# Kernel optimization log

Measured on AMD Instinct MI355X. Metric: run time of the kernel, lower is better.

The kernel has to match this reference:

```python
import jax, jax.numpy as jnp
import numpy as np


def setup_inputs() -> dict:
    key = jax.random.key(0)
    k1, k2, k3, k4 = jax.random.split(key, 4)
    B, S, D = 2, 2048, 1024
    return {
        "X": jax.random.normal(k1, (B, S, D), dtype=jnp.float32),
        "W_q": jax.random.normal(k2, (D, D), dtype=jnp.float32),
        "W_k": jax.random.normal(k3, (D, D), dtype=jnp.float32),
        "W_v": jax.random.normal(k4, (D, D), dtype=jnp.float32),
        "n_heads": 16,
    }


def reference(X, W_q, W_k, W_v, n_heads):
    B, S, D = X.shape
    H = n_heads
    dh = D // H
    # QKV projections, split heads: [B,S,D] -> [H,B,S,dh]
    def split_heads(Y):
        return Y.reshape(B, S, H, dh).transpose(2, 0, 1, 3)
    Q = split_heads(X @ W_q)
    K = split_heads(X @ W_k)
    V = split_heads(X @ W_v)
    scale = 1.0 / jnp.sqrt(jnp.asarray(dh, dtype=X.dtype))
    # [H,B,S,S] attention scores (naive, matches the original)
    scores = jax.nn.softmax(jnp.einsum("hbqd,hbkd->hbqk", Q, K) * scale, axis=-1)
    out = jnp.einsum("hbqk,hbkd->hbqd", scores, V)  # [H,B,S,dh]
    # torch.concat(out, 0) over leading H dim -> [H*B, S, dh]
    return out.reshape(H * B, S, dh)
```

## Files before the change

### kernel.cpp

```cpp
#include <hip/hip_runtime.h>

typedef unsigned short u16;
typedef unsigned int u32;
typedef __bf16 bf16x8 __attribute__((ext_vector_type(8)));
typedef float f32x4 __attribute__((ext_vector_type(4)));

#define WT_HI_E  ((size_t)0)
#define WT_LO_E  ((size_t)3 << 20)
#define X_HI_E   ((size_t)6 << 20)
#define X_LO_E   ((size_t)10 << 20)
#define Q_HI_E   ((size_t)14 << 20)
#define Q_LO_E   ((size_t)18 << 20)
#define K_HI_E   ((size_t)22 << 20)
#define K_LO_E   ((size_t)26 << 20)
#define V_HI_E   ((size_t)30 << 20)

__device__ __forceinline__ u16 bf16_rne(float x) {
  u32 u = __float_as_uint(x);
  u32 r = (u + 0x7fffu + ((u >> 16) & 1u)) >> 16;
  return (u16)r;
}
__device__ __forceinline__ float bf16_f(u16 h) {
  return __uint_as_float(((u32)h) << 16);
}

__device__ __forceinline__ void gload16(const u16* g, u16* l) {
  __builtin_amdgcn_global_load_lds(
      (const __attribute__((address_space(1))) void*)g,
      (__attribute__((address_space(3))) void*)l, 16, 0, 0);
}

__global__ __launch_bounds__(256) void k_xsplit(const float* __restrict__ X,
                                                u16* __restrict__ ws) {
  u16* xh = ws + X_HI_E;
  u16* xl = ws + X_LO_E;
  size_t i = ((size_t)blockIdx.x * 256 + threadIdx.x) * 8;
  float4 a = *(const float4*)(X + i);
  float4 b = *(const float4*)(X + i + 4);
  float v[8] = {a.x, a.y, a.z, a.w, b.x, b.y, b.z, b.w};
  u32 Hh[4], Ll[4];
#pragma unroll
  for (int j = 0; j < 4; j++) {
    u16 h0 = bf16_rne(v[2 * j]);
    u16 l0 = bf16_rne(v[2 * j] - bf16_f(h0));
    u16 h1 = bf16_rne(v[2 * j + 1]);
    u16 l1 = bf16_rne(v[2 * j + 1] - bf16_f(h1));
    Hh[j] = (u32)h0 | ((u32)h1 << 16);
    Ll[j] = (u32)l0 | ((u32)l1 << 16);
  }
  *(uint4*)(xh + i) = make_uint4(Hh[0], Hh[1], Hh[2], Hh[3]);
  *(uint4*)(xl + i) = make_uint4(Ll[0], Ll[1], Ll[2], Ll[3]);
}

__global__ __launch_bounds__(256) void k_wsplit(const float* __restrict__ w0,
                                                const float* __restrict__ w1,
                                                const float* __restrict__ w2,
                                                u16* __restrict__ ws) {
  int z = blockIdx.z;
  const float* W = (z == 0) ? w0 : ((z == 1) ? w1 : w2);
  u16* th = ws + WT_HI_E + (size_t)z * (1u << 20);
  u16* tl = ws + WT_LO_E + (size_t)z * (1u << 20);
  __shared__ float tile[32][33];
  int bx = blockIdx.x * 32, by = blockIdx.y * 32;
  int tx = threadIdx.x & 31, ty = threadIdx.x >> 5;
#pragma unroll
  for (int i = 0; i < 4; i++) {
    int r = ty + i * 8;
    tile[r][tx] = W[(size_t)(by + r) * 1024 + bx + tx];
  }
  __syncthreads();
#pragma unroll
  for (int i = 0; i < 4; i++) {
    int r = ty + i * 8;
    float v = tile[tx][r];
    int n = bx + r, k = by + tx;
    u16 h = bf16_rne(v);
    u16 l = bf16_rne(v - bf16_f(h));
    th[(size_t)n * 1024 + k] = h;
    tl[(size_t)n * 1024 + k] = l;
  }
}

__global__ __launch_bounds__(256) void k_proj(u16* __restrict__ ws) {
  int z = blockIdx.z;
  const u16* Xh = ws + X_HI_E;
  const u16* Xl = ws + X_LO_E;
  const u16* Wh = ws + WT_HI_E + (size_t)z * (1u << 20);
  const u16* Wl = ws + WT_LO_E + (size_t)z * (1u << 20);
  u16* dsth = ws + ((z == 0) ? Q_HI_E : ((z == 1) ? K_HI_E : V_HI_E));
  u16* dstl = (z == 0) ? (ws + Q_LO_E) : ((z == 1) ? (ws + K_LO_E) : (u16*)0);

  __shared__ u16 sXh[4096], sXl[4096], sWh[4096], sWl[4096];
  int M0 = blockIdx.y * 128, N0 = blockIdx.x * 128;
  int tid = threadIdx.x, lane = tid & 63, w = tid >> 6;
  int quad = lane >> 4, l16 = lane & 15;
  int mb = (w & 1) * 64, nb = (w >> 1) * 64;

  const f32x4 z4 = {0.f, 0.f, 0.f, 0.f};
  f32x4 acc[4][4];
#pragma unroll
  for (int i = 0; i < 4; i++)
#pragma unroll
    for (int j = 0; j < 4; j++) acc[i][j] = z4;

  for (int kk = 0; kk < 1024; kk += 32) {
    __syncthreads();
#pragma unroll
    for (int c2 = 0; c2 < 2; c2++) {
      int cb = c2 * 256 + w * 64;
      int c = cb + lane;
      int row = c >> 2, q8 = c & 3;
      size_t gx = (size_t)(M0 + row) * 1024 + kk + q8 * 8;
      size_t gw = (size_t)(N0 + row) * 1024 + kk + q8 * 8;
      gload16(Xh + gx, sXh + (size_t)cb * 8);
      gload16(Wh + gw, sWh + (size_t)cb * 8);
      if (z != 2) {
        gload16(Xl + gx, sXl + (size_t)cb * 8);
        gload16(Wl + gw, sWl + (size_t)cb * 8);
      }
    }
    __syncthreads();
    bf16x8 ah[4], bh[4];
#pragma unroll
    for (int i = 0; i < 4; i++) {
      ah[i] = *(const bf16x8*)&sXh[(mb + i * 16 + l16) * 32 + quad * 8];
      bh[i] = *(const bf16x8*)&sWh[(nb + i * 16 + l16) * 32 + quad * 8];
    }
    if (z != 2) {
      bf16x8 al[4], bl[4];
#pragma unroll
      for (int i = 0; i < 4; i++) {
        al[i] = *(const bf16x8*)&sXl[(mb + i * 16 + l16) * 32 + quad * 8];
        bl[i] = *(const bf16x8*)&sWl[(nb + i * 16 + l16) * 32 + quad * 8];
      }
#pragma unroll
      for (int i = 0; i < 4; i++)
#pragma unroll
        for (int j = 0; j < 4; j++) {
          f32x4 c0 = acc[i][j];
          c0 = __builtin_amdgcn_mfma_f32_16x16x32_bf16(ah[i], bh[j], c0, 0, 0, 0);
          c0 = __builtin_amdgcn_mfma_f32_16x16x32_bf16(ah[i], bl[j], c0, 0, 0, 0);
          c0 = __builtin_amdgcn_mfma_f32_16x16x32_bf16(al[i], bh[j], c0, 0, 0, 0);
          acc[i][j] = c0;
        }
    } else {
#pragma unroll
      for (int i = 0; i < 4; i++)
#pragma unroll
        for (int j = 0; j < 4; j++)
          acc[i][j] = __builtin_amdgcn_mfma_f32_16x16x32_bf16(ah[i], bh[j], acc[i][j], 0, 0, 0);
    }
  }

  if (z == 2) {
#pragma unroll
    for (int i = 0; i < 4; i++)
#pragma unroll
      for (int j = 0; j < 4; j++) {
        int mg = M0 + mb + i * 16 + quad * 4;
        int ng = N0 + nb + j * 16 + l16;
        int b = mg >> 11, s = mg & 2047;
        int hh = ng >> 6, d = ng & 63;
        u16 p0 = bf16_rne(acc[i][j][0]);
        u16 p1 = bf16_rne(acc[i][j][1]);
        u16 p2 = bf16_rne(acc[i][j][2]);
        u16 p3 = bf16_rne(acc[i][j][3]);
        *(uint2*)&dsth[((size_t)(hh * 2 + b) * 64 + d) * 2048 + s] =
            make_uint2((u32)p0 | ((u32)p1 << 16), (u32)p2 | ((u32)p3 << 16));
      }
  } else {
    float qscale = (z == 0) ? 0.125f : 1.0f;
#pragma unroll
    for (int i = 0; i < 4; i++)
#pragma unroll
      for (int j = 0; j < 4; j++)
#pragma unroll
        for (int r = 0; r < 4; r++) {
          int mg = M0 + mb + i * 16 + quad * 4 + r;
          int ng = N0 + nb + j * 16 + l16;
          int b = mg >> 11, s = mg & 2047;
          int hh = ng >> 6, d = ng & 63;
          size_t idx = ((size_t)(hh * 2 + b) * 2048 + s) * 64 + d;
          float y = acc[i][j][r] * qscale;
          u16 h = bf16_rne(y);
          dsth[idx] = h;
          dstl[idx] = bf16_rne(y - bf16_f(h));
        }
  }
}

__global__ __launch_bounds__(256, 4) void k_attn(u16* __restrict__ ws,
                                                 float* __restrict__ out) {
  const u16* Qh = ws + Q_HI_E;
  const u16* Ql = ws + Q_LO_E;
  const u16* Kh = ws + K_HI_E;
  const u16* Kl = ws + K_LO_E;
  const u16* Vt = ws + V_HI_E;

  __shared__ u16 sKh[2][64][32], sKl[2][64][32], sVt[2][64][32];
  __shared__ u16 sP[4][16][72];

  int id = blockIdx.x;
  int hb = id & 31, qb = id >> 5;
  int q0 = qb * 64;

  int tid = threadIdx.x, w = tid >> 6, lane = tid & 63;
  int quad = lane >> 4, l16 = lane & 15;
  size_t base = (size_t)hb * (2048 * 64);
  int row0 = q0 + w * 16;

  bf16x8 qh[2], ql[2];
#pragma unroll
  for (int kc = 0; kc < 2; kc++) {
    size_t off = base + (size_t)(row0 + l16) * 64 + kc * 32 + quad * 8;
    qh[kc] = *(const bf16x8*)(Qh + off);
    ql[kc] = *(const bf16x8*)(Ql + off);
  }
  const f32x4 z4 = {0.f, 0.f, 0.f, 0.f};
  float mr = -1e30f, lr = 0.f;
  f32x4 o[4];
#pragma unroll
  for (int dn = 0; dn < 4; dn++) o[dn] = z4;

  int srow = w * 16 + (lane >> 2);
  int sch = lane & 3;

  for (int kt = 0; kt < 2048; kt += 64) {
    __syncthreads();
#pragma unroll
    for (int kc = 0; kc < 2; kc++) {
      size_t kg = base + (size_t)(kt + srow) * 64 + kc * 32 + sch * 8;
      gload16(Kh + kg, &sKh[kc][w * 16][0]);
      gload16(Kl + kg, &sKl[kc][w * 16][0]);
      size_t vg = base + (size_t)srow * 2048 + kt + kc * 32 + sch * 8;
      gload16(Vt + vg, &sVt[kc][w * 16][0]);
    }
    __syncthreads();

    f32x4 sc[4] = {z4, z4, z4, z4};
#pragma unroll
    for (int kc = 0; kc < 2; kc++) {
      bf16x8 kh[4], klo[4];
#pragma unroll
      for (int nt = 0; nt < 4; nt++) {
        kh[nt] = *(const bf16x8*)&sKh[kc][nt * 16 + l16][quad * 8];
        klo[nt] = *(const bf16x8*)&sKl[kc][nt * 16 + l16][quad * 8];
      }
#pragma unroll
      for (int nt = 0; nt < 4; nt++) {
        f32x4 a = sc[nt];
        a = __builtin_amdgcn_mfma_f32_16x16x32_bf16(kh[nt], qh[kc], a, 0, 0, 0);
        a = __builtin_amdgcn_mfma_f32_16x16x32_bf16(kh[nt], ql[kc], a, 0, 0, 0);
        a = __builtin_amdgcn_mfma_f32_16x16x32_bf16(klo[nt], qh[kc], a, 0, 0, 0);
        sc[nt] = a;
      }
    }
    float m1v = sc[0][0];
#pragma unroll
    for (int nt = 0; nt < 4; nt++)
#pragma unroll
      for (int r = 0; r < 4; r++) m1v = fmaxf(m1v, sc[nt][r]);
    m1v = fmaxf(m1v, __shfl_xor(m1v, 16));
    m1v = fmaxf(m1v, __shfl_xor(m1v, 32));
    float mnew = fmaxf(mr, m1v);
    float alpha = __expf(mr - mnew);
    mr = mnew;
    float rs = 0.f;
#pragma unroll
    for (int nt = 0; nt < 4; nt++) {
      float p0 = __expf(sc[nt][0] - mnew);
      float p1 = __expf(sc[nt][1] - mnew);
      float p2 = __expf(sc[nt][2] - mnew);
      float p3 = __expf(sc[nt][3] - mnew);
      rs += (p0 + p1) + (p2 + p3);
      *(uint2*)&sP[w][l16][nt * 16 + quad * 4] =
          make_uint2((u32)bf16_rne(p0) | ((u32)bf16_rne(p1) << 16),
                     (u32)bf16_rne(p2) | ((u32)bf16_rne(p3) << 16));
    }
    rs += __shfl_xor(rs, 16);
    rs += __shfl_xor(rs, 32);
    lr = lr * alpha + rs;
    float af[4];
#pragma unroll
    for (int r = 0; r < 4; r++) af[r] = __shfl(alpha, quad * 20 + r);
#pragma unroll
    for (int dn = 0; dn < 4; dn++)
#pragma unroll
      for (int r = 0; r < 4; r++) o[dn][r] *= af[r];
#pragma unroll
    for (int kc = 0; kc < 2; kc++) {
      bf16x8 pa = *(const bf16x8*)&sP[w][l16][kc * 32 + quad * 8];
#pragma unroll
      for (int dn = 0; dn < 4; dn++) {
        bf16x8 vb = *(const bf16x8*)&sVt[kc][dn * 16 + l16][quad * 8];
        o[dn] = __builtin_amdgcn_mfma_f32_16x16x32_bf16(pa, vb, o[dn], 0, 0, 0);
      }
    }
  }

  float lf[4];
#pragma unroll
  for (int r = 0; r < 4; r++) lf[r] = __shfl(lr, quad * 20 + r);
#pragma unroll
  for (int r = 0; r < 4; r++) {
    int row = row0 + quad * 4 + r;
    size_t g = (size_t)hb * 2048 + row;
    float inv = 1.f / lf[r];
#pragma unroll
    for (int dn = 0; dn < 4; dn++) out[g * 64 + dn * 16 + l16] = o[dn][r] * inv;
  }
}

extern "C" void kernel_launch(void* const* d_in, const int* in_sizes, int n_in,
                              void* d_out, int out_size, void* d_ws, size_t ws_size,
                              hipStream_t stream) {
  const float* X = (const float*)d_in[0];
  const float* Wq = (const float*)d_in[1];
  const float* Wk = (const float*)d_in[2];
  const float* Wv = (const float*)d_in[3];
  u16* ws = (u16*)d_ws;
  float* out = (float*)d_out;

  k_xsplit<<<dim3(2048), dim3(256), 0, stream>>>(X, ws);
  k_wsplit<<<dim3(32, 32, 3), dim3(256), 0, stream>>>(Wq, Wk, Wv, ws);
  k_proj<<<dim3(8, 32, 3), dim3(256), 0, stream>>>(ws);
  k_attn<<<dim3(1024), dim3(256), 0, stream>>>(ws, out);
}
```

Baseline: 263.6 us.

## Rework attention kernel with 32x32 MFMA, swizzled K/V layout and double-buffered staging

The attention kernel now gives each wave 32 query rows and uses 32x32x16 MFMA tiles, doubling the query tile per block and halving the grid. The probability tile stays in registers, exchanged between lane halves with cross-lane shuffles, so the shared-memory round trip for P goes away. K/V tiles are double-buffered so the next tile's loads overlap compute, and one barrier per iteration remains. The projection kernel writes K and V^T in an XOR-swizzled layout to avoid LDS bank conflicts on reads. The trade-offs are higher register pressure (launch bounds lowered to 2 blocks/SM), fewer blocks, and P rounding done by simple add-and-truncate.

```diff
diff --git a/kernel.cpp b/kernel.cpp
--- a/kernel.cpp
+++ b/kernel.cpp
@@ -4,6 +4,7 @@
 typedef unsigned int u32;
 typedef __bf16 bf16x8 __attribute__((ext_vector_type(8)));
 typedef float f32x4 __attribute__((ext_vector_type(4)));
+typedef float f32x16 __attribute__((ext_vector_type(16)));
 
 #define WT_HI_E  ((size_t)0)
 #define WT_LO_E  ((size_t)3 << 20)
@@ -161,11 +162,13 @@
         int ng = N0 + nb + j * 16 + l16;
         int b = mg >> 11, s = mg & 2047;
         int hh = ng >> 6, d = ng & 63;
+        int cp = ((s >> 3) & 7) ^ (d & 7);
+        int ssw = (s & ~63) | (cp << 3) | (s & 7);
         u16 p0 = bf16_rne(acc[i][j][0]);
         u16 p1 = bf16_rne(acc[i][j][1]);
         u16 p2 = bf16_rne(acc[i][j][2]);
         u16 p3 = bf16_rne(acc[i][j][3]);
-        *(uint2*)&dsth[((size_t)(hh * 2 + b) * 64 + d) * 2048 + s] =
+        *(uint2*)&dsth[((size_t)(hh * 2 + b) * 64 + d) * 2048 + ssw] =
             make_uint2((u32)p0 | ((u32)p1 << 16), (u32)p2 | ((u32)p3 << 16));
       }
   } else {
@@ -180,7 +183,9 @@
           int ng = N0 + nb + j * 16 + l16;
           int b = mg >> 11, s = mg & 2047;
           int hh = ng >> 6, d = ng & 63;
-          size_t idx = ((size_t)(hh * 2 + b) * 2048 + s) * 64 + d;
+          int d2 = d;
+          if (z == 1) d2 = ((((d >> 3) ^ (s & 7)) & 7) << 3) | (d & 7);
+          size_t idx = ((size_t)(hh * 2 + b) * 2048 + s) * 64 + d2;
           float y = acc[i][j][r] * qscale;
           u16 h = bf16_rne(y);
           dsth[idx] = h;
@@ -189,7 +194,7 @@
   }
 }
 
-__global__ __launch_bounds__(256, 4) void k_attn(u16* __restrict__ ws,
+__global__ __launch_bounds__(256, 2) void k_attn(u16* __restrict__ ws,
                                                  float* __restrict__ out) {
   const u16* Qh = ws + Q_HI_E;
   const u16* Ql = ws + Q_LO_E;
@@ -197,118 +202,127 @@
   const u16* Kl = ws + K_LO_E;
   const u16* Vt = ws + V_HI_E;
 
-  __shared__ u16 sKh[2][64][32], sKl[2][64][32], sVt[2][64][32];
-  __shared__ u16 sP[4][16][72];
+  __shared__ u16 sKh[2][64][64], sKl[2][64][64], sVt[2][64][64];
 
   int id = blockIdx.x;
   int hb = id & 31, qb = id >> 5;
-  int q0 = qb * 64;
-
   int tid = threadIdx.x, w = tid >> 6, lane = tid & 63;
-  int quad = lane >> 4, l16 = lane & 15;
+  int l31 = lane & 31, h = lane >> 5;
   size_t base = (size_t)hb * (2048 * 64);
-  int row0 = q0 + w * 16;
-
-  bf16x8 qh[2], ql[2];
-#pragma unroll
-  for (int kc = 0; kc < 2; kc++) {
-    size_t off = base + (size_t)(row0 + l16) * 64 + kc * 32 + quad * 8;
-    qh[kc] = *(const bf16x8*)(Qh + off);
-    ql[kc] = *(const bf16x8*)(Ql + off);
-  }
-  const f32x4 z4 = {0.f, 0.f, 0.f, 0.f};
+  int qw0 = qb * 128 + w * 32;
+
+  int srow = lane >> 3, sch = lane & 7;
+
+  auto stage = [&](int buf, int kt) {
+#pragma unroll
+    for (int b2 = 0; b2 < 2; b2++) {
+      int rr = w * 16 + b2 * 8;
+      size_t kg = base + (size_t)(kt + rr + srow) * 64 + sch * 8;
+      gload16(Kh + kg, &sKh[buf][rr][0]);
+      gload16(Kl + kg, &sKl[buf][rr][0]);
+      size_t vg = base + (size_t)(rr + srow) * 2048 + kt + sch * 8;
+      gload16(Vt + vg, &sVt[buf][rr][0]);
+    }
+  };
+
+  stage(0, 0);
+
+  bf16x8 qh[4], ql[4];
+#pragma unroll
+  for (int ks = 0; ks < 4; ks++) {
+    size_t off = base + (size_t)(qw0 + l31) * 64 + ks * 16 + h * 8;
+    qh[ks] = *(const bf16x8*)(Qh + off);
+    ql[ks] = *(const bf16x8*)(Ql + off);
+  }
+
+  f32x16 o[2];
+#pragma unroll
+  for (int i = 0; i < 16; i++) { o[0][i] = 0.f; o[1][i] = 0.f; }
   float mr = -1e30f, lr = 0.f;
-  f32x4 o[4];
-#pragma unroll
-  for (int dn = 0; dn < 4; dn++) o[dn] = z4;
-
-  int srow = w * 16 + (lane >> 2);
-  int sch = lane & 3;
-
-  for (int kt = 0; kt < 2048; kt += 64) {
+
+  auto rdA = [&](const u16 t[64][64], int mt, int ks) -> bf16x8 {
+    int ch = ((ks * 2 + h) ^ (l31 & 7)) * 8;
+    return *(const bf16x8*)&t[mt * 32 + l31][ch];
+  };
+
+  for (int it = 0; it < 32; it++) {
     __syncthreads();
-#pragma unroll
-    for (int kc = 0; kc < 2; kc++) {
-      size_t kg = base + (size_t)(kt + srow) * 64 + kc * 32 + sch * 8;
-      gload16(Kh + kg, &sKh[kc][w * 16][0]);
-      gload16(Kl + kg, &sKl[kc][w * 16][0]);
-      size_t vg = base + (size_t)srow * 2048 + kt + kc * 32 + sch * 8;
-      gload16(Vt + vg, &sVt[kc][w * 16][0]);
-    }
-    __syncthreads();
-
-    f32x4 sc[4] = {z4, z4, z4, z4};
-#pragma unroll
-    for (int kc = 0; kc < 2; kc++) {
-      bf16x8 kh[4], klo[4];
-#pragma unroll
-      for (int nt = 0; nt < 4; nt++) {
-        kh[nt] = *(const bf16x8*)&sKh[kc][nt * 16 + l16][quad * 8];
-        klo[nt] = *(const bf16x8*)&sKl[kc][nt * 16 + l16][quad * 8];
-      }
-#pragma unroll
-      for (int nt = 0; nt < 4; nt++) {
-        f32x4 a = sc[nt];
-        a = __builtin_amdgcn_mfma_f32_16x16x32_bf16(kh[nt], qh[kc], a, 0, 0, 0);
-        a = __builtin_amdgcn_mfma_f32_16x16x32_bf16(kh[nt], ql[kc], a, 0, 0, 0);
-        a = __builtin_amdgcn_mfma_f32_16x16x32_bf16(klo[nt], qh[kc], a, 0, 0, 0);
-        sc[nt] = a;
-      }
-    }
-    float m1v = sc[0][0];
-#pragma unroll
-    for (int nt = 0; nt < 4; nt++)
-#pragma unroll
-      for (int r = 0; r < 4; r++) m1v = fmaxf(m1v, sc[nt][r]);
-    m1v = fmaxf(m1v, __shfl_xor(m1v, 16));
-    m1v = fmaxf(m1v, __shfl_xor(m1v, 32));
-    float mnew = fmaxf(mr, m1v);
+    if (it + 1 < 32) stage((it + 1) & 1, (it + 1) * 64);
+    int buf = it & 1;
+
+    f32x16 sc[2];
+#pragma unroll
+    for (int i = 0; i < 16; i++) { sc[0][i] = 0.f; sc[1][i] = 0.f; }
+#pragma unroll
+    for (int ks = 0; ks < 4; ks++)
+#pragma unroll
+      for (int mt = 0; mt < 2; mt++) {
+        bf16x8 kh = rdA(sKh[buf], mt, ks);
+        bf16x8 kl = rdA(sKl[buf], mt, ks);
+        sc[mt] = __builtin_amdgcn_mfma_f32_32x32x16_bf16(kh, qh[ks], sc[mt], 0, 0, 0);
+        sc[mt] = __builtin_amdgcn_mfma_f32_32x32x16_bf16(kh, ql[ks], sc[mt], 0, 0, 0);
+        sc[mt] = __builtin_amdgcn_mfma_f32_32x32x16_bf16(kl, qh[ks], sc[mt], 0, 0, 0);
+      }
+
+    float mx = sc[0][0];
+#pragma unroll
+    for (int i = 0; i < 16; i++) {
+      mx = fmaxf(mx, sc[0][i]);
+      mx = fmaxf(mx, sc[1][i]);
+    }
+    mx = fmaxf(mx, __shfl_xor(mx, 32));
+    float mnew = fmaxf(mr, mx);
     float alpha = __expf(mr - mnew);
     mr = mnew;
     float rs = 0.f;
-#pragma unroll
-    for (int nt = 0; nt < 4; nt++) {
-      float p0 = __expf(sc[nt][0] - mnew);
-      float p1 = __expf(sc[nt][1] - mnew);
-      float p2 = __expf(sc[nt][2] - mnew);
-      float p3 = __expf(sc[nt][3] - mnew);
-      rs += (p0 + p1) + (p2 + p3);
-      *(uint2*)&sP[w][l16][nt * 16 + quad * 4] =
-          make_uint2((u32)bf16_rne(p0) | ((u32)bf16_rne(p1) << 16),
-                     (u32)bf16_rne(p2) | ((u32)bf16_rne(p3) << 16));
-    }
-    rs += __shfl_xor(rs, 16);
+    u32 pk[2][8];
+#pragma unroll
+    for (int t = 0; t < 2; t++)
+#pragma unroll
+      for (int i = 0; i < 8; i++) {
+        float p0 = __expf(sc[t][2 * i] - mnew);
+        float p1 = __expf(sc[t][2 * i + 1] - mnew);
+        rs += p0 + p1;
+        u32 a = __float_as_uint(p0) + 0x8000u;
+        u32 b = __float_as_uint(p1) + 0x8000u;
+        pk[t][i] = __builtin_amdgcn_perm(b, a, 0x07060302u);
+      }
     rs += __shfl_xor(rs, 32);
     lr = lr * alpha + rs;
-    float af[4];
-#pragma unroll
-    for (int r = 0; r < 4; r++) af[r] = __shfl(alpha, quad * 20 + r);
-#pragma unroll
-    for (int dn = 0; dn < 4; dn++)
-#pragma unroll
-      for (int r = 0; r < 4; r++) o[dn][r] *= af[r];
-#pragma unroll
-    for (int kc = 0; kc < 2; kc++) {
-      bf16x8 pa = *(const bf16x8*)&sP[w][l16][kc * 32 + quad * 8];
-#pragma unroll
-      for (int dn = 0; dn < 4; dn++) {
-        bf16x8 vb = *(const bf16x8*)&sVt[kc][dn * 16 + l16][quad * 8];
-        o[dn] = __builtin_amdgcn_mfma_f32_16x16x32_bf16(pa, vb, o[dn], 0, 0, 0);
-      }
-    }
-  }
-
-  float lf[4];
-#pragma unroll
-  for (int r = 0; r < 4; r++) lf[r] = __shfl(lr, quad * 20 + r);
-#pragma unroll
-  for (int r = 0; r < 4; r++) {
-    int row = row0 + quad * 4 + r;
-    size_t g = (size_t)hb * 2048 + row;
-    float inv = 1.f / lf[r];
-#pragma unroll
-    for (int dn = 0; dn < 4; dn++) out[g * 64 + dn * 16 + l16] = o[dn][r] * inv;
-  }
+#pragma unroll
+    for (int i = 0; i < 16; i++) {
+      o[0][i] *= alpha;
+      o[1][i] *= alpha;
+    }
+
+#pragma unroll
+    for (int ks = 0; ks < 4; ks++) {
+      int t = ks >> 1, c = ks & 1;
+      u32 b0 = pk[t][c * 4 + 0], b1 = pk[t][c * 4 + 1];
+      u32 b2 = pk[t][c * 4 + 2], b3 = pk[t][c * 4 + 3];
+      u32 rA = (u32)__shfl_xor((int)(h ? b0 : b2), 32);
+      u32 rB = (u32)__shfl_xor((int)(h ? b1 : b3), 32);
+      uint4 fb = h ? make_uint4(rA, rB, b2, b3) : make_uint4(b0, b1, rA, rB);
+      bf16x8 pfrag = *(bf16x8*)&fb;
+#pragma unroll
+      for (int mt = 0; mt < 2; mt++) {
+        bf16x8 vb = rdA(sVt[buf], mt, ks);
+        o[mt] = __builtin_amdgcn_mfma_f32_32x32x16_bf16(vb, pfrag, o[mt], 0, 0, 0);
+      }
+    }
+  }
+
+  float inv = 1.f / lr;
+  size_t grow = (size_t)hb * 2048 + qw0 + l31;
+#pragma unroll
+  for (int mt = 0; mt < 2; mt++)
+#pragma unroll
+    for (int g2 = 0; g2 < 4; g2++) {
+      int d0 = mt * 32 + g2 * 8 + 4 * h;
+      float4 v = make_float4(o[mt][g2 * 4 + 0] * inv, o[mt][g2 * 4 + 1] * inv,
+                             o[mt][g2 * 4 + 2] * inv, o[mt][g2 * 4 + 3] * inv);
+      *(float4*)(out + grow * 64 + d0) = v;
+    }
 }
 
 extern "C" void kernel_launch(void* const* d_in, const int* in_sizes, int n_in,
@@ -324,5 +338,5 @@
   k_xsplit<<<dim3(2048), dim3(256), 0, stream>>>(X, ws);
   k_wsplit<<<dim3(32, 32, 3), dim3(256), 0, stream>>>(Wq, Wk, Wv, ws);
   k_proj<<<dim3(8, 32, 3), dim3(256), 0, stream>>>(ws);
-  k_attn<<<dim3(1024), dim3(256), 0, stream>>>(ws, out);
-}
+  k_attn<<<dim3(512), dim3(256), 0, stream>>>(ws, out);
+}
```

After: 243.3 us. -7.7%, faster.
